# Kernel optimization log

Measured on AMD Instinct MI355X. Metric: run time of the kernel, lower is better.

The kernel has to match this reference:

```python
import jax, jax.numpy as jnp
import numpy as np

B, DIM, NUM_HEADS = 16384, 2048, 4
SD = DIM // 2            # single_dim = 1024
HD = SD // NUM_HEADS     # head_dim = 256
LH = SD // 4             # lambda-net hidden = 256
SCALE = HD ** -0.5


def setup_inputs() -> dict:
    key = jax.random.key(0)
    ks = jax.random.split(key, 20)
    w = lambda k, shape: jax.random.normal(k, shape, dtype=jnp.float32) * 0.02
    inp = {
        "x": jax.random.normal(ks[0], (B, DIM), dtype=jnp.float32),
        # Linear weights stored (in, out); y = x @ W + b (equivalent to torch Linear)
        "WQ1_w": w(ks[1], (SD, SD)), "WQ1_b": jnp.zeros((SD,), jnp.float32),
        "WK1_w": w(ks[2], (SD, SD)), "WK1_b": jnp.zeros((SD,), jnp.float32),
        "WQ2_w": w(ks[3], (SD, SD)), "WQ2_b": jnp.zeros((SD,), jnp.float32),
        "WK2_w": w(ks[4], (SD, SD)), "WK2_b": jnp.zeros((SD,), jnp.float32),
        "WV_w": w(ks[5], (SD, SD)), "WV_b": jnp.zeros((SD,), jnp.float32),
        "WO_w": w(ks[6], (SD, SD)), "WO_b": jnp.zeros((SD,), jnp.float32),
        "L1_w": w(ks[7], (DIM, LH)), "L1_b": jnp.zeros((LH,), jnp.float32),
        "L2_w": w(ks[8], (LH, 1)), "L2_b": jnp.zeros((1,), jnp.float32),
    }
    return inp


def _heads(t, W, b):
    # tokens [B,2,SD] -> [B,H,2,HD]
    y = t @ W + b
    return y.reshape(B, 2, NUM_HEADS, HD).transpose(0, 2, 1, 3)


def reference(x, WQ1_w, WQ1_b, WK1_w, WK1_b, WQ2_w, WQ2_b, WK2_w, WK2_b,
              WV_w, WV_b, WO_w, WO_b, L1_w, L1_b, L2_w, L2_b):
    tokens = x.reshape(B, 2, SD)
    # gating lambda in (0,1): MLP(x) -> [B,1,1,1]
    lam = jax.nn.sigmoid(jax.nn.relu(x @ L1_w + L1_b) @ L2_w + L2_b)
    lam = lam.reshape(B, 1, 1, 1)

    Q1 = _heads(tokens, WQ1_w, WQ1_b)
    K1 = _heads(tokens, WK1_w, WK1_b)
    Q2 = _heads(tokens, WQ2_w, WQ2_b)
    K2 = _heads(tokens, WK2_w, WK2_b)
    V = _heads(tokens, WV_w, WV_b)

    attn1 = jax.nn.softmax(jnp.einsum("bhqd,bhkd->bhqk", Q1, K1) * SCALE, axis=-1)
    attn2 = jax.nn.softmax(jnp.einsum("bhqd,bhkd->bhqk", Q2, K2) * SCALE, axis=-1)
    diff_attn = jax.nn.relu(attn1 - lam * attn2)  # dropout = identity (eval)

    out = jnp.einsum("bhqk,bhkd->bhqd", diff_attn, V)  # [B,H,2,HD]
    out = out.transpose(0, 2, 1, 3).reshape(B, 2, SD)
    out = (out @ WO_w + WO_b) + tokens
    return out.reshape(B, SD * 2)
```

## Files before the change

kernel.cpp:

```cpp
#include <hip/hip_runtime.h>
#include <stdint.h>


#define BATCH  16384
#define ATT_SCALE 0.0625f

typedef __attribute__((ext_vector_type(8)))  short   s16x8;
typedef __attribute__((ext_vector_type(4)))  float   f32x4;
typedef __attribute__((ext_vector_type(2)))  float   f32x2;
typedef __attribute__((ext_vector_type(8)))  int     i32x8;
typedef __attribute__((ext_vector_type(8)))  unsigned short u16x8;
typedef __attribute__((ext_vector_type(4)))  unsigned short u16x4;

__device__ __forceinline__ unsigned short f2bf(float f) {
  unsigned u = __float_as_uint(f);
  u += 0x7FFFu + ((u >> 16) & 1u);
  return (unsigned short)(u >> 16);
}
__device__ __forceinline__ float bf2f(unsigned short s) {
  return __uint_as_float((unsigned)s << 16);
}

__device__ __forceinline__ unsigned char f2e4m3(float f) {
  unsigned u = __float_as_uint(f);
  unsigned s = (u >> 24) & 0x80u;
  float a = fabsf(f);
  if (a >= 448.f) return (unsigned char)(s | 0x7E);
  if (a < 0.0009765625f) return (unsigned char)s;
  int e = (int)((u >> 23) & 0xFF) - 127;
  if (e < -6) {
    int q = (int)rintf(a * 512.f);
    if (q >= 8) return (unsigned char)(s | 0x08);
    return (unsigned char)(s | q);
  }
  unsigned mant = u & 0x7FFFFFu;
  unsigned mr = mant + 0x7FFFFu + ((mant >> 20) & 1u);
  e += (int)(mr >> 23);
  mant = (mr >> 20) & 7u;
  if (e > 8) return (unsigned char)(s | 0x7E);
  return (unsigned char)(s | ((e + 7) << 3) | mant);
}
__device__ __forceinline__ float e4m3f(unsigned v) {
  unsigned e = (v >> 3) & 15u, m = v & 7u;
  float mag = (e == 0) ? (float)m * 0.001953125f
                       : __uint_as_float(((e + 120u) << 23) | (m << 20));
  return (v & 0x80u) ? -mag : mag;
}

__device__ __forceinline__ unsigned char cvt1_fp8(float v) {
#if __has_builtin(__builtin_amdgcn_cvt_pk_fp8_f32)
  return (unsigned char)(__builtin_amdgcn_cvt_pk_fp8_f32(v, v, 0, false) & 0xff);
#else
  return f2e4m3(v);
#endif
}

__device__ __forceinline__ void dec8(uint2 p, float* o) {
#if __has_builtin(__builtin_amdgcn_cvt_pk_f32_fp8)
  f32x2 a = __builtin_amdgcn_cvt_pk_f32_fp8((int)p.x, false);
  f32x2 b = __builtin_amdgcn_cvt_pk_f32_fp8((int)p.x, true);
  f32x2 c = __builtin_amdgcn_cvt_pk_f32_fp8((int)p.y, false);
  f32x2 d = __builtin_amdgcn_cvt_pk_f32_fp8((int)p.y, true);
  o[0] = a[0]; o[1] = a[1]; o[2] = b[0]; o[3] = b[1];
  o[4] = c[0]; o[5] = c[1]; o[6] = d[0]; o[7] = d[1];
#else
#pragma unroll
  for (int j = 0; j < 4; ++j) o[j]     = e4m3f((p.x >> (8 * j)) & 255u);
#pragma unroll
  for (int j = 0; j < 4; ++j) o[4 + j] = e4m3f((p.y >> (8 * j)) & 255u);
#endif
}

__device__ __forceinline__ void async16(const void* g, void* l) {
  __builtin_amdgcn_global_load_lds((__attribute__((address_space(1))) void*)g,
                                   (__attribute__((address_space(3))) void*)l,
                                   16, 0, 0);
}

__global__ __launch_bounds__(512, 2)
void gemm_mx(const unsigned char* __restrict__ A,
             const unsigned char* __restrict__ Bt,
             const float* __restrict__ bias,
             unsigned char* __restrict__ Cout,
             int NN)
{
  __shared__ __align__(16) char lds[131072];
  const int tid  = threadIdx.x;
  const int lane = tid & 63, w = tid >> 6;
  const int wm = w >> 2, wn = w & 3;
  const int li = lane & 15, lc = lane >> 4;

  const int nwg = gridDim.x;
  const int swz = (blockIdx.x & 7) * (nwg >> 3) + (blockIdx.x >> 3);
  const int bm = (swz / NN) * 256;
  const int bn = (swz % NN) * 256;

  const int grow   = lane >> 3;
  const int gchunk = ((lane & 7) ^ grow) * 16;
  size_t aSrc[4], bSrc[4];
  int dstKB[4];
#pragma unroll
  for (int i = 0; i < 4; ++i) {
    const int rr = (i * 8 + w) * 8 + grow;
    aSrc[i] = (size_t)(bm + rr) * 1024 + gchunk;
    bSrc[i] = (size_t)(bn + rr) * 1024 + gchunk;
    dstKB[i] = (i * 8 + w) * 1024;
  }

  const int x7   = li & 7;
  const int off0 = ((2 * lc)     ^ x7) * 16;
  const int off1 = ((2 * lc + 1) ^ x7) * 16;
  const int aRow = (wm * 128 + li) * 128;
  const int bRow = 32768 + (wn * 64 + li) * 128;

  f32x4 acc[8][4];
#pragma unroll
  for (int m = 0; m < 8; ++m)
#pragma unroll
    for (int n = 0; n < 4; ++n) acc[m][n] = (f32x4)0.f;

#pragma unroll
  for (int i = 0; i < 4; ++i) {
    async16(A  + aSrc[i], lds + dstKB[i]);
    async16(Bt + bSrc[i], lds + 32768 + dstKB[i]);
  }
#pragma unroll
  for (int i = 0; i < 4; ++i) {
    async16(A  + aSrc[i] + 128, lds + 65536 + dstKB[i]);
    async16(Bt + bSrc[i] + 128, lds + 98304 + dstKB[i]);
  }
  asm volatile("s_waitcnt vmcnt(8)" ::: "memory");
  __builtin_amdgcn_s_barrier();

  for (int t = 0; t < 8; ++t) {
    char* buf = lds + (t & 1) * 65536;
    const char* ab = buf;
    const char* bb = buf;

    i32x8 bF[4];
#pragma unroll
    for (int nf = 0; nf < 4; ++nf) {
      const char* p = bb + bRow + nf * 2048;
      uint4 h0 = *(const uint4*)(p + off0);
      uint4 h1 = *(const uint4*)(p + off1);
      bF[nf][0] = h0.x; bF[nf][1] = h0.y; bF[nf][2] = h0.z; bF[nf][3] = h0.w;
      bF[nf][4] = h1.x; bF[nf][5] = h1.y; bF[nf][6] = h1.z; bF[nf][7] = h1.w;
    }
#pragma unroll
    for (int mh = 0; mh < 2; ++mh) {
      i32x8 aF[4];
#pragma unroll
      for (int mf = 0; mf < 4; ++mf) {
        const char* p = ab + aRow + (mh * 4 + mf) * 2048;
        uint4 h0 = *(const uint4*)(p + off0);
        uint4 h1 = *(const uint4*)(p + off1);
        aF[mf][0] = h0.x; aF[mf][1] = h0.y; aF[mf][2] = h0.z; aF[mf][3] = h0.w;
        aF[mf][4] = h1.x; aF[mf][5] = h1.y; aF[mf][6] = h1.z; aF[mf][7] = h1.w;
      }
      __builtin_amdgcn_s_setprio(1);
#pragma unroll
      for (int mf = 0; mf < 4; ++mf)
#pragma unroll
        for (int nf = 0; nf < 4; ++nf)
          acc[mh * 4 + mf][nf] = __builtin_amdgcn_mfma_scale_f32_16x16x128_f8f6f4(
              aF[mf], bF[nf], acc[mh * 4 + mf][nf],
              0, 0,
              0, 0x7F7F7F7F,
              0, 0x7F7F7F7F);
      __builtin_amdgcn_s_setprio(0);
    }
    __builtin_amdgcn_s_barrier();
    if (t + 2 < 8) {
      const size_t kt = (size_t)(t + 2) * 128;
#pragma unroll
      for (int i = 0; i < 4; ++i) {
        async16(A  + aSrc[i] + kt, buf + dstKB[i]);
        async16(Bt + bSrc[i] + kt, buf + 32768 + dstKB[i]);
      }
    }
    if (t < 6) { asm volatile("s_waitcnt vmcnt(8)" ::: "memory"); }
    else       { asm volatile("s_waitcnt vmcnt(0)" ::: "memory"); }
    __builtin_amdgcn_s_barrier();
  }

  float bv[4];
#pragma unroll
  for (int n = 0; n < 4; ++n) bv[n] = bias[bn + wn * 64 + n * 16 + li];

  unsigned char* wl0 = (unsigned char*)(lds + w * 12288);
#pragma unroll
  for (int mp = 0; mp < 4; ++mp) {
    unsigned char* wl = wl0 + (mp & 1) * 2560;
#pragma unroll
    for (int mi = 0; mi < 2; ++mi)
#pragma unroll
      for (int n = 0; n < 4; ++n)
#pragma unroll
        for (int jj = 0; jj < 4; ++jj) {
          float v = acc[mp * 2 + mi][n][jj] + bv[n];
          wl[(mi * 16 + lc * 4 + jj) * 80 + n * 16 + li] = cvt1_fp8(v);
        }
    const size_t base = (size_t)((bm + wm * 128 + mp * 32) >> 5) * 131072
                      + (size_t)((bn >> 6) + wn) * 2048;
    uint4 v0 = *(const uint4*)(wl + (lane >> 2) * 80 + (lane & 3) * 16);
    *(uint4*)(Cout + base + lane * 16) = v0;
    uint4 v1 = *(const uint4*)(wl + (16 + (lane >> 2)) * 80 + (lane & 3) * 16);
    *(uint4*)(Cout + base + 1024 + lane * 16) = v1;
  }
}

template<int MODE>
__global__ __launch_bounds__(512, 2)
void gemm256(const unsigned short* __restrict__ A,
             const unsigned short* __restrict__ Bt,
             const float* __restrict__ bias,
             void* __restrict__ Cout,
             const unsigned short* __restrict__ res,
             int Kdim, int Ndim, int NN,
             const unsigned short* __restrict__ lamBt,
             const float* __restrict__ lamL1b,
             const float* __restrict__ lamL2w,
             float* __restrict__ lamp)
{
  __shared__ __align__(16) char lds[131072];
  const int tid  = threadIdx.x;
  const int lane = tid & 63, w = tid >> 6;
  const int wm = w >> 2, wn = w & 3;
  const int li = lane & 15, lc = lane >> 4;

  if (MODE == 4 && blockIdx.x < 128) {
    const int bm_l = blockIdx.x * 128;
    const int t = tid;
    const size_t aSrc  = (size_t)(bm_l + (t >> 2)) * 2048 + (t & 3) * 8;
    const size_t b0Src = (size_t)(t >> 2) * 2048 + (t & 3) * 8;
    const size_t b1Src = (size_t)(128 + (t >> 2)) * 2048 + (t & 3) * 8;

    f32x4 acc[4][4];
#pragma unroll
    for (int i = 0; i < 4; ++i)
#pragma unroll
      for (int j = 0; j < 4; ++j) acc[i][j] = (f32x4)0.f;

    for (int k0 = 0; k0 < 2048; k0 += 32) {
      async16(A     + aSrc  + k0, lds + w * 1024);
      async16(lamBt + b0Src + k0, lds + 8192 + w * 1024);
      async16(lamBt + b1Src + k0, lds + 16384 + w * 1024);
      __syncthreads();
      s16x8 aR[4], bR[4];
#pragma unroll
      for (int m = 0; m < 4; ++m)
        aR[m] = *(const s16x8*)(lds + ((w >> 2) * 64 + m * 16 + li) * 64 + lc * 16);
#pragma unroll
      for (int n = 0; n < 4; ++n)
        bR[n] = *(const s16x8*)(lds + 8192 + ((w & 3) * 64 + n * 16 + li) * 64 + lc * 16);
#pragma unroll
      for (int m = 0; m < 4; ++m)
#pragma unroll
        for (int n = 0; n < 4; ++n)
          acc[m][n] = __builtin_amdgcn_mfma_f32_16x16x32_bf16(aR[m], bR[n], acc[m][n], 0, 0, 0);
      __syncthreads();
    }

    float l2v[4], bvv[4];
#pragma unroll
    for (int n = 0; n < 4; ++n) {
      const int col = (w & 3) * 64 + n * 16 + li;
      l2v[n] = lamL2w[col];
      bvv[n] = lamL1b[col];
    }
#pragma unroll
    for (int m = 0; m < 4; ++m)
#pragma unroll
      for (int j = 0; j < 4; ++j) {
        float part = 0.f;
#pragma unroll
        for (int n = 0; n < 4; ++n)
          part += fmaxf(acc[m][n][j] + bvv[n], 0.f) * l2v[n];
        part += __shfl_xor(part, 1, 64);
        part += __shfl_xor(part, 2, 64);
        part += __shfl_xor(part, 4, 64);
        part += __shfl_xor(part, 8, 64);
        if ((lane & 15) == 0)
          atomicAdd(lamp + bm_l + (w >> 2) * 64 + m * 16 + lc * 4 + j, part);
      }
    return;
  }

  int bid, nwg;
  if (MODE == 4) { bid = blockIdx.x - 128; nwg = 512; }
  else           { bid = blockIdx.x;       nwg = gridDim.x; }
  const int q8 = nwg >> 3, r8 = nwg & 7;
  const int xcd = bid & 7, pos = bid >> 3;
  const int swz = (xcd < r8 ? xcd * (q8 + 1) : r8 * (q8 + 1) + (xcd - r8) * q8) + pos;
  const int bm = (swz / NN) * 256;
  const int bn = (swz % NN) * 256;

  const int r0  = w * 32 + (lane >> 2);
  const int csw = ((lane & 3) ^ ((r0 >> 1) & 3)) * 8;
  const size_t aS0 = (size_t)(bm + r0) * Kdim + csw;
  const size_t aS1 = (size_t)(bm + r0 + 16) * Kdim + csw;
  const size_t bS0 = (size_t)(bn + r0) * Kdim + csw;
  const size_t bS1 = (size_t)(bn + r0 + 16) * Kdim + csw;
  const int dL0 = w * 2048, dL1 = dL0 + 1024;

  const int fsw   = (lc ^ ((li >> 1) & 3)) << 4;
  const int afoff = (wm * 128 + li) * 64 + fsw;
  const int bfoff = 32768 + (wn * 64 + li) * 64 + fsw;

  f32x4 acc[8][4];
#pragma unroll
  for (int m = 0; m < 8; ++m)
#pragma unroll
    for (int n = 0; n < 4; ++n) acc[m][n] = (f32x4)0.f;

  const int NT = Kdim >> 6;

  async16(A  + aS0,       lds + dL0);          async16(A  + aS1,       lds + dL1);
  async16(Bt + bS0,       lds + 32768 + dL0);  async16(Bt + bS1,       lds + 32768 + dL1);
  async16(A  + aS0 + 32,  lds + 16384 + dL0);  async16(A  + aS1 + 32,  lds + 16384 + dL1);
  async16(Bt + bS0 + 32,  lds + 49152 + dL0);  async16(Bt + bS1 + 32,  lds + 49152 + dL1);
  async16(A  + aS0 + 64,  lds + 65536 + dL0);  async16(A  + aS1 + 64,  lds + 65536 + dL1);
  async16(Bt + bS0 + 64,  lds + 98304 + dL0);  async16(Bt + bS1 + 64,  lds + 98304 + dL1);
  asm volatile("s_waitcnt vmcnt(4)" ::: "memory");
  __builtin_amdgcn_s_barrier();

  for (int t = 0; t < NT; ++t) {
    char* buf  = lds + (t & 1) * 65536;
    char* nbuf = lds + ((t + 1) & 1) * 65536;
    const size_t kA = (size_t)t * 64;
    const bool s1 = (t + 1 < NT), s2 = (t + 2 < NT);
    s16x8 a0[4], a1[4], bR[4];

    {
      const char* ab = buf + afoff;
      const char* bb = buf + bfoff;
#pragma unroll
      for (int i = 0; i < 4; ++i) a0[i] = *(const s16x8*)(ab + i * 1024);
#pragma unroll
      for (int i = 0; i < 4; ++i) a1[i] = *(const s16x8*)(ab + 4096 + i * 1024);
#pragma unroll
      for (int i = 0; i < 4; ++i) bR[i] = *(const s16x8*)(bb + i * 1024);
      if (s1) {
        async16(A  + aS0 + kA + 96, nbuf + 16384 + dL0);
        async16(A  + aS1 + kA + 96, nbuf + 16384 + dL1);
        async16(Bt + bS0 + kA + 96, nbuf + 49152 + dL0);
        async16(Bt + bS1 + kA + 96, nbuf + 49152 + dL1);
      }
      __builtin_amdgcn_s_setprio(1);
#pragma unroll
      for (int mf = 0; mf < 4; ++mf)
#pragma unroll
        for (int nf = 0; nf < 4; ++nf) {
          acc[mf][nf]     = __builtin_amdgcn_mfma_f32_16x16x32_bf16(a0[mf], bR[nf], acc[mf][nf], 0, 0, 0);
          acc[4 + mf][nf] = __builtin_amdgcn_mfma_f32_16x16x32_bf16(a1[mf], bR[nf], acc[4 + mf][nf], 0, 0, 0);
        }
      __builtin_amdgcn_s_setprio(0);
      __builtin_amdgcn_s_barrier();
    }
    {
      const char* ab = buf + 16384 + afoff;
      const char* bb = buf + 16384 + bfoff;
#pragma unroll
      for (int i = 0; i < 4; ++i) a0[i] = *(const s16x8*)(ab + i * 1024);
#pragma unroll
      for (int i = 0; i < 4; ++i) a1[i] = *(const s16x8*)(ab + 4096 + i * 1024);
#pragma unroll
      for (int i = 0; i < 4; ++i) bR[i] = *(const s16x8*)(bb + i * 1024);
      if (s2) {
        async16(A  + aS0 + kA + 128, buf + dL0);
        async16(A  + aS1 + kA + 128, buf + dL1);
        async16(Bt + bS0 + kA + 128, buf + 32768 + dL0);
        async16(Bt + bS1 + kA + 128, buf + 32768 + dL1);
      }
      __builtin_amdgcn_s_setprio(1);
#pragma unroll
      for (int mf = 0; mf < 4; ++mf)
#pragma unroll
        for (int nf = 0; nf < 4; ++nf) {
          acc[mf][nf]     = __builtin_amdgcn_mfma_f32_16x16x32_bf16(a0[mf], bR[nf], acc[mf][nf], 0, 0, 0);
          acc[4 + mf][nf] = __builtin_amdgcn_mfma_f32_16x16x32_bf16(a1[mf], bR[nf], acc[4 + mf][nf], 0, 0, 0);
        }
      __builtin_amdgcn_s_setprio(0);
      if (t < NT - 2)       { asm volatile("s_waitcnt vmcnt(4)" ::: "memory"); }
      else if (t == NT - 2) { asm volatile("s_waitcnt vmcnt(0)" ::: "memory"); }
      __builtin_amdgcn_s_barrier();
    }
  }

  float bv[4];
#pragma unroll
  for (int n = 0; n < 4; ++n) bv[n] = bias[bn + wn * 64 + n * 16 + li];

  if (MODE == 4) {
    unsigned short* Cv = (unsigned short*)Cout;
    unsigned short* wl0 = (unsigned short*)(lds + w * 12288);
#pragma unroll
    for (int mp = 0; mp < 4; ++mp) {
      unsigned short* wl = wl0 + (mp & 1) * 2304;
#pragma unroll
      for (int mi = 0; mi < 2; ++mi)
#pragma unroll
        for (int n = 0; n < 4; ++n)
#pragma unroll
          for (int jj = 0; jj < 4; ++jj) {
            float v = acc[mp * 2 + mi][n][jj] + bv[n];
            wl[(mi * 16 + lc * 4 + jj) * 72 + li + n * 16] = f2bf(v);
          }
#pragma unroll
      for (int i = 0; i < 4; ++i) {
        const int rr = i * 8 + (lane >> 3);
        u16x8 vv = *(const u16x8*)(wl + rr * 72 + (lane & 7) * 8);
        const size_t gi = (size_t)(bm + wm * 128 + mp * 32 + rr) * 1024
                        + bn + wn * 64 + (lane & 7) * 8;
        *(u16x8*)(Cv + gi) = vv;
      }
    }
  } else {
    float* Cf = (float*)Cout;
    float* wl0 = (float*)(lds + w * 12288);
#pragma unroll
    for (int m = 0; m < 8; ++m) {
      float* wl = wl0 + (m & 1) * 1088;
#pragma unroll
      for (int n = 0; n < 4; ++n)
#pragma unroll
        for (int jj = 0; jj < 4; ++jj)
          wl[(lc * 4 + jj) * 68 + li + n * 16] = acc[m][n][jj] + bv[n];
#pragma unroll
      for (int i = 0; i < 4; ++i) {
        const int rr = i * 4 + lc;
        f32x4 vv = *(const f32x4*)(wl + rr * 68 + li * 4);
        const size_t gi = (size_t)(bm + wm * 128 + m * 16 + rr) * Ndim
                        + bn + wn * 64 + li * 4;
        const u16x4 rv = *(const u16x4*)(res + gi);
        f32x4 ov;
#pragma unroll
        for (int jj = 0; jj < 4; ++jj) ov[jj] = vv[jj] + bf2f(rv[jj]);
        *(f32x4*)(Cf + gi) = ov;
      }
    }
  }
}

__global__ __launch_bounds__(256)
void attn_kernel(const unsigned char* __restrict__ qk8,
                 const unsigned short* __restrict__ vbuf,
                 const float* __restrict__ lam_pre,
                 const float* __restrict__ L2b,
                 unsigned short* __restrict__ aout)
{
  const int b = blockIdx.x;
  const int hd = threadIdx.x >> 6;
  const int lane = threadIdx.x & 63;
  const int g = lane >> 5;
  const int l5 = lane & 31;
  const size_t row = (size_t)(2 * b + g);

  const size_t cbase = (row >> 5) * 131072
                     + (size_t)(hd * 4 + (l5 >> 3)) * 2048
                     + (row & 31) * 64 + (l5 & 7) * 8;
  const uint2 p1 = *(const uint2*)(qk8 + cbase);
  const uint2 p2 = *(const uint2*)(qk8 + cbase + 32768);
  const uint2 p3 = *(const uint2*)(qk8 + cbase + 65536);
  const uint2 p4 = *(const uint2*)(qk8 + cbase + 98304);
  const u16x8 vvv = *(const u16x8*)(vbuf + row * 1024 + hd * 256 + l5 * 8);

  float q1[8], k1[8], q2[8], k2[8], vf[8];
  dec8(p1, q1); dec8(p2, k1); dec8(p3, q2); dec8(p4, k2);
#pragma unroll
  for (int j = 0; j < 8; ++j) vf[j] = bf2f(vvv[j]);

  float ss1 = 0.f, sc1 = 0.f, ss2 = 0.f, sc2 = 0.f;
#pragma unroll
  for (int j = 0; j < 8; ++j) {
    const float k1o = __shfl_xor(k1[j], 32, 64);
    const float k2o = __shfl_xor(k2[j], 32, 64);
    ss1 += q1[j] * k1[j]; sc1 += q1[j] * k1o;
    ss2 += q2[j] * k2[j]; sc2 += q2[j] * k2o;
  }
#pragma unroll
  for (int m = 16; m >= 1; m >>= 1) {
    ss1 += __shfl_xor(ss1, m, 64); sc1 += __shfl_xor(sc1, m, 64);
    ss2 += __shfl_xor(ss2, m, 64); sc2 += __shfl_xor(sc2, m, 64);
  }

  float e0 = ss1 * ATT_SCALE, e1 = sc1 * ATT_SCALE;
  float mx = fmaxf(e0, e1);
  float xs = expf(e0 - mx), xc = expf(e1 - mx);
  float inv = 1.f / (xs + xc);
  const float a1s = xs * inv, a1c = xc * inv;

  e0 = ss2 * ATT_SCALE; e1 = sc2 * ATT_SCALE;
  mx = fmaxf(e0, e1);
  xs = expf(e0 - mx); xc = expf(e1 - mx);
  inv = 1.f / (xs + xc);
  const float a2s = xs * inv, a2c = xc * inv;

  const float lm = 1.f / (1.f + expf(-(lam_pre[b] + L2b[0])));
  const float ps = fmaxf(a1s - lm * a2s, 0.f);
  const float pc = fmaxf(a1c - lm * a2c, 0.f);

  u16x8 o;
#pragma unroll
  for (int j = 0; j < 8; ++j) {
    const float vo = __shfl_xor(vf[j], 32, 64);
    o[j] = f2bf(ps * vf[j] + pc * vo);
  }
  *(u16x8*)(aout + row * 1024 + hd * 256 + l5 * 8) = o;
}

__global__ void prep_k(const float* __restrict__ s0, const float* __restrict__ s1,
                       const float* __restrict__ s2, const float* __restrict__ s3,
                       const float* __restrict__ s4, const float* __restrict__ s5,
                       const float* __restrict__ L1w,
                       const float* __restrict__ b0, const float* __restrict__ b1,
                       const float* __restrict__ b2, const float* __restrict__ b3,
                       const float* __restrict__ b4,
                       const float* __restrict__ x,
                       unsigned char* __restrict__ qw8,
                       unsigned short* __restrict__ vw,
                       unsigned short* __restrict__ wot,
                       unsigned short* __restrict__ l1t,
                       float* __restrict__ bcat,
                       unsigned short* __restrict__ x_bf,
                       unsigned char* __restrict__ x_f8,
                       float* __restrict__ lamp)
{
  __shared__ float tile[32][33];
  const int z = blockIdx.z;
  const int tx = threadIdx.x, ty = threadIdx.y;

  if (z < 6) {
    const float* W;
    switch (z) {
      case 0: W = s0; break;
      case 1: W = s1; break;
      case 2: W = s2; break;
      case 3: W = s3; break;
      case 4: W = s4; break;
      default: W = s5; break;
    }
    const int bn = blockIdx.x * 32, bk = blockIdx.y * 32;
#pragma unroll
    for (int i = ty; i < 32; i += 8)
      tile[i][tx] = W[(size_t)(bk + i) * 1024 + bn + tx];
    __syncthreads();
    if (z < 4) {
      unsigned char* Wt = qw8 + (size_t)z * 1048576;
#pragma unroll
      for (int i = ty; i < 32; i += 8)
        Wt[(size_t)(bn + i) * 1024 + bk + tx] = cvt1_fp8(tile[tx][i]);
    } else {
      unsigned short* Wt = (z == 4) ? vw : wot;
#pragma unroll
      for (int i = ty; i < 32; i += 8)
        Wt[(size_t)(bn + i) * 1024 + bk + tx] = f2bf(tile[tx][i]);
    }
    return;
  }
  if (z < 22) {
    const int c = (z - 6) * 1024 + blockIdx.y * 32 + blockIdx.x;
    const int i = c * 256 + ty * 32 + tx;
    const float4* p = (const float4*)x + (size_t)i * 2;
    float4 a = p[0], b = p[1];
    float f[8] = {a.x, a.y, a.z, a.w, b.x, b.y, b.z, b.w};
    u16x8 v; unsigned lo = 0, hi = 0;
#pragma unroll
    for (int j = 0; j < 8; ++j) v[j] = f2bf(f[j]);
#pragma unroll
    for (int j = 0; j < 4; ++j) lo |= (unsigned)cvt1_fp8(f[j]) << (8 * j);
#pragma unroll
    for (int j = 0; j < 4; ++j) hi |= (unsigned)cvt1_fp8(f[4 + j]) << (8 * j);
    *(u16x8*)(x_bf + (size_t)i * 8) = v;
    uint2 c8; c8.x = lo; c8.y = hi;
    *(uint2*)(x_f8 + (size_t)i * 8) = c8;
    return;
  }
  if (z == 22) {
    const int idx = blockIdx.y * 32 + blockIdx.x;
    if (idx >= 512) return;
    const int bn = (idx & 7) * 32, bk = (idx >> 3) * 32;
#pragma unroll
    for (int i = ty; i < 32; i += 8)
      tile[i][tx] = L1w[(size_t)(bk + i) * 256 + bn + tx];
    __syncthreads();
#pragma unroll
    for (int i = ty; i < 32; i += 8)
      l1t[(size_t)(bn + i) * 2048 + bk + tx] = f2bf(tile[tx][i]);
    return;
  }
  const int idx = blockIdx.y * 32 + blockIdx.x;
  const int t = ty * 32 + tx;
  if (idx < 20) {
    const int i = idx * 256 + t;
    const float* src;
    switch (i >> 10) {
      case 0: src = b0; break;
      case 1: src = b1; break;
      case 2: src = b2; break;
      case 3: src = b3; break;
      default: src = b4; break;
    }
    bcat[i] = src[i & 1023];
  } else if (idx < 84) {
    lamp[(idx - 20) * 256 + t] = 0.f;
  }
}

extern "C" void kernel_launch(void* const* d_in, const int* in_sizes, int n_in,
                              void* d_out, int out_size, void* d_ws, size_t ws_size,
                              hipStream_t stream)
{
  const float* x    = (const float*)d_in[0];
  const float* WQ1w = (const float*)d_in[1];  const float* WQ1b = (const float*)d_in[2];
  const float* WK1w = (const float*)d_in[3];  const float* WK1b = (const float*)d_in[4];
  const float* WQ2w = (const float*)d_in[5];  const float* WQ2b = (const float*)d_in[6];
  const float* WK2w = (const float*)d_in[7];  const float* WK2b = (const float*)d_in[8];
  const float* WVw  = (const float*)d_in[9];  const float* WVb  = (const float*)d_in[10];
  const float* WOw  = (const float*)d_in[11]; const float* WOb  = (const float*)d_in[12];
  const float* L1w  = (const float*)d_in[13]; const float* L1b  = (const float*)d_in[14];
  const float* L2w  = (const float*)d_in[15]; const float* L2b  = (const float*)d_in[16];

  char* ws = (char*)d_ws;
  size_t off = 0;
  unsigned short* x_bf = (unsigned short*)(ws + off); off += (size_t)33554432 * 2;
  unsigned char*  x_f8 = (unsigned char*)(ws + off);  off += (size_t)33554432;
  unsigned char*  qw8  = (unsigned char*)(ws + off);  off += (size_t)4194304;
  unsigned short* vw   = (unsigned short*)(ws + off); off += (size_t)1048576 * 2;
  unsigned short* wot  = (unsigned short*)(ws + off); off += (size_t)1048576 * 2;
  unsigned short* l1t  = (unsigned short*)(ws + off); off += (size_t)524288 * 2;
  float*          bcat = (float*)(ws + off);          off += (size_t)5120 * 4;
  unsigned char*  qk8  = (unsigned char*)(ws + off);  off += (size_t)32768 * 4096;
  unsigned short* vbuf = (unsigned short*)(ws + off); off += (size_t)33554432 * 2;
  unsigned short* abuf = (unsigned short*)(ws + off); off += (size_t)33554432 * 2;
  float*          lamp = (float*)(ws + off);          off += (size_t)16384 * 4;

  prep_k<<<dim3(32, 32, 24), dim3(32, 8), 0, stream>>>(
      WQ1w, WK1w, WQ2w, WK2w, WVw, WOw, L1w,
      WQ1b, WK1b, WQ2b, WK2b, WVb, x,
      qw8, vw, wot, l1t, bcat, x_bf, x_f8, lamp);

  gemm_mx<<<dim3(2048), 512, 0, stream>>>(x_f8, qw8, bcat, qk8, 16);

  gemm256<4><<<dim3(128 + 512), 512, 0, stream>>>(
      x_bf, vw, bcat + 4096, vbuf, nullptr, 1024, 1024, 4, l1t, L1b, L2w, lamp);

  attn_kernel<<<16384, 256, 0, stream>>>(qk8, vbuf, lamp, L2b, abuf);

  gemm256<2><<<dim3(512), 512, 0, stream>>>(
      abuf, wot, WOb, d_out, x_bf, 1024, 1024, 4, nullptr, nullptr, nullptr, nullptr);
}
```

Before: 467.9 us.

## Compute V projection in FP8 MFMA, merged into QK GEMM launch with lambda net

The V projection weight is now quantized to FP8 with the Q/K weights, so V comes out of the same FP8 scaled-MFMA GEMM as Q1/K1/Q2/K2 (N widened from 4096 to 5120), written back as bf16. The lambda-MLP blocks move into this combined launch, which drops one kernel launch and replaces the bf16 V GEMM with the cheaper FP8 path. In exchange V loses precision from FP8 inputs, which may hurt accuracy. The output projection becomes its own non-templated kernel.

```diff
diff --git a/kernel.cpp b/kernel.cpp
--- a/kernel.cpp
+++ b/kernel.cpp
@@ -82,141 +82,9 @@
              const unsigned char* __restrict__ Bt,
              const float* __restrict__ bias,
              unsigned char* __restrict__ Cout,
-             int NN)
-{
-  __shared__ __align__(16) char lds[131072];
-  const int tid  = threadIdx.x;
-  const int lane = tid & 63, w = tid >> 6;
-  const int wm = w >> 2, wn = w & 3;
-  const int li = lane & 15, lc = lane >> 4;
-
-  const int nwg = gridDim.x;
-  const int swz = (blockIdx.x & 7) * (nwg >> 3) + (blockIdx.x >> 3);
-  const int bm = (swz / NN) * 256;
-  const int bn = (swz % NN) * 256;
-
-  const int grow   = lane >> 3;
-  const int gchunk = ((lane & 7) ^ grow) * 16;
-  size_t aSrc[4], bSrc[4];
-  int dstKB[4];
-#pragma unroll
-  for (int i = 0; i < 4; ++i) {
-    const int rr = (i * 8 + w) * 8 + grow;
-    aSrc[i] = (size_t)(bm + rr) * 1024 + gchunk;
-    bSrc[i] = (size_t)(bn + rr) * 1024 + gchunk;
-    dstKB[i] = (i * 8 + w) * 1024;
-  }
-
-  const int x7   = li & 7;
-  const int off0 = ((2 * lc)     ^ x7) * 16;
-  const int off1 = ((2 * lc + 1) ^ x7) * 16;
-  const int aRow = (wm * 128 + li) * 128;
-  const int bRow = 32768 + (wn * 64 + li) * 128;
-
-  f32x4 acc[8][4];
-#pragma unroll
-  for (int m = 0; m < 8; ++m)
-#pragma unroll
-    for (int n = 0; n < 4; ++n) acc[m][n] = (f32x4)0.f;
-
-#pragma unroll
-  for (int i = 0; i < 4; ++i) {
-    async16(A  + aSrc[i], lds + dstKB[i]);
-    async16(Bt + bSrc[i], lds + 32768 + dstKB[i]);
-  }
-#pragma unroll
-  for (int i = 0; i < 4; ++i) {
-    async16(A  + aSrc[i] + 128, lds + 65536 + dstKB[i]);
-    async16(Bt + bSrc[i] + 128, lds + 98304 + dstKB[i]);
-  }
-  asm volatile("s_waitcnt vmcnt(8)" ::: "memory");
-  __builtin_amdgcn_s_barrier();
-
-  for (int t = 0; t < 8; ++t) {
-    char* buf = lds + (t & 1) * 65536;
-    const char* ab = buf;
-    const char* bb = buf;
-
-    i32x8 bF[4];
-#pragma unroll
-    for (int nf = 0; nf < 4; ++nf) {
-      const char* p = bb + bRow + nf * 2048;
-      uint4 h0 = *(const uint4*)(p + off0);
-      uint4 h1 = *(const uint4*)(p + off1);
-      bF[nf][0] = h0.x; bF[nf][1] = h0.y; bF[nf][2] = h0.z; bF[nf][3] = h0.w;
-      bF[nf][4] = h1.x; bF[nf][5] = h1.y; bF[nf][6] = h1.z; bF[nf][7] = h1.w;
-    }
-#pragma unroll
-    for (int mh = 0; mh < 2; ++mh) {
-      i32x8 aF[4];
-#pragma unroll
-      for (int mf = 0; mf < 4; ++mf) {
-        const char* p = ab + aRow + (mh * 4 + mf) * 2048;
-        uint4 h0 = *(const uint4*)(p + off0);
-        uint4 h1 = *(const uint4*)(p + off1);
-        aF[mf][0] = h0.x; aF[mf][1] = h0.y; aF[mf][2] = h0.z; aF[mf][3] = h0.w;
-        aF[mf][4] = h1.x; aF[mf][5] = h1.y; aF[mf][6] = h1.z; aF[mf][7] = h1.w;
-      }
-      __builtin_amdgcn_s_setprio(1);
-#pragma unroll
-      for (int mf = 0; mf < 4; ++mf)
-#pragma unroll
-        for (int nf = 0; nf < 4; ++nf)
-          acc[mh * 4 + mf][nf] = __builtin_amdgcn_mfma_scale_f32_16x16x128_f8f6f4(
-              aF[mf], bF[nf], acc[mh * 4 + mf][nf],
-              0, 0,
-              0, 0x7F7F7F7F,
-              0, 0x7F7F7F7F);
-      __builtin_amdgcn_s_setprio(0);
-    }
-    __builtin_amdgcn_s_barrier();
-    if (t + 2 < 8) {
-      const size_t kt = (size_t)(t + 2) * 128;
-#pragma unroll
-      for (int i = 0; i < 4; ++i) {
-        async16(A  + aSrc[i] + kt, buf + dstKB[i]);
-        async16(Bt + bSrc[i] + kt, buf + 32768 + dstKB[i]);
-      }
-    }
-    if (t < 6) { asm volatile("s_waitcnt vmcnt(8)" ::: "memory"); }
-    else       { asm volatile("s_waitcnt vmcnt(0)" ::: "memory"); }
-    __builtin_amdgcn_s_barrier();
-  }
-
-  float bv[4];
-#pragma unroll
-  for (int n = 0; n < 4; ++n) bv[n] = bias[bn + wn * 64 + n * 16 + li];
-
-  unsigned char* wl0 = (unsigned char*)(lds + w * 12288);
-#pragma unroll
-  for (int mp = 0; mp < 4; ++mp) {
-    unsigned char* wl = wl0 + (mp & 1) * 2560;
-#pragma unroll
-    for (int mi = 0; mi < 2; ++mi)
-#pragma unroll
-      for (int n = 0; n < 4; ++n)
-#pragma unroll
-        for (int jj = 0; jj < 4; ++jj) {
-          float v = acc[mp * 2 + mi][n][jj] + bv[n];
-          wl[(mi * 16 + lc * 4 + jj) * 80 + n * 16 + li] = cvt1_fp8(v);
-        }
-    const size_t base = (size_t)((bm + wm * 128 + mp * 32) >> 5) * 131072
-                      + (size_t)((bn >> 6) + wn) * 2048;
-    uint4 v0 = *(const uint4*)(wl + (lane >> 2) * 80 + (lane & 3) * 16);
-    *(uint4*)(Cout + base + lane * 16) = v0;
-    uint4 v1 = *(const uint4*)(wl + (16 + (lane >> 2)) * 80 + (lane & 3) * 16);
-    *(uint4*)(Cout + base + 1024 + lane * 16) = v1;
-  }
-}
-
-template<int MODE>
-__global__ __launch_bounds__(512, 2)
-void gemm256(const unsigned short* __restrict__ A,
-             const unsigned short* __restrict__ Bt,
-             const float* __restrict__ bias,
-             void* __restrict__ Cout,
-             const unsigned short* __restrict__ res,
-             int Kdim, int Ndim, int NN,
+             unsigned short* __restrict__ Vout,
+             int NN,
+             const unsigned short* __restrict__ xbf,
              const unsigned short* __restrict__ lamBt,
              const float* __restrict__ lamL1b,
              const float* __restrict__ lamL2w,
@@ -228,7 +96,7 @@
   const int wm = w >> 2, wn = w & 3;
   const int li = lane & 15, lc = lane >> 4;
 
-  if (MODE == 4 && blockIdx.x < 128) {
+  if (blockIdx.x < 128) {
     const int bm_l = blockIdx.x * 128;
     const int t = tid;
     const size_t aSrc  = (size_t)(bm_l + (t >> 2)) * 2048 + (t & 3) * 8;
@@ -242,7 +110,7 @@
       for (int j = 0; j < 4; ++j) acc[i][j] = (f32x4)0.f;
 
     for (int k0 = 0; k0 < 2048; k0 += 32) {
-      async16(A     + aSrc  + k0, lds + w * 1024);
+      async16(xbf   + aSrc  + k0, lds + w * 1024);
       async16(lamBt + b0Src + k0, lds + 8192 + w * 1024);
       async16(lamBt + b1Src + k0, lds + 16384 + w * 1024);
       __syncthreads();
@@ -286,11 +154,165 @@
     return;
   }
 
-  int bid, nwg;
-  if (MODE == 4) { bid = blockIdx.x - 128; nwg = 512; }
-  else           { bid = blockIdx.x;       nwg = gridDim.x; }
+  const int bid = blockIdx.x - 128;
+  const int nwg = 2560;
+  const int swz = (bid & 7) * (nwg >> 3) + (bid >> 3);
+  const int bm = (swz / NN) * 256;
+  const int bn = (swz % NN) * 256;
+
+  const int grow   = lane >> 3;
+  const int gchunk = ((lane & 7) ^ grow) * 16;
+  size_t aSrc[4], bSrc[4];
+  int dstKB[4];
+#pragma unroll
+  for (int i = 0; i < 4; ++i) {
+    const int rr = (i * 8 + w) * 8 + grow;
+    aSrc[i] = (size_t)(bm + rr) * 1024 + gchunk;
+    bSrc[i] = (size_t)(bn + rr) * 1024 + gchunk;
+    dstKB[i] = (i * 8 + w) * 1024;
+  }
+
+  const int x7   = li & 7;
+  const int off0 = ((2 * lc)     ^ x7) * 16;
+  const int off1 = ((2 * lc + 1) ^ x7) * 16;
+  const int aRow = (wm * 128 + li) * 128;
+  const int bRow = 32768 + (wn * 64 + li) * 128;
+
+  f32x4 acc[8][4];
+#pragma unroll
+  for (int m = 0; m < 8; ++m)
+#pragma unroll
+    for (int n = 0; n < 4; ++n) acc[m][n] = (f32x4)0.f;
+
+#pragma unroll
+  for (int i = 0; i < 4; ++i) {
+    async16(A  + aSrc[i], lds + dstKB[i]);
+    async16(Bt + bSrc[i], lds + 32768 + dstKB[i]);
+  }
+#pragma unroll
+  for (int i = 0; i < 4; ++i) {
+    async16(A  + aSrc[i] + 128, lds + 65536 + dstKB[i]);
+    async16(Bt + bSrc[i] + 128, lds + 98304 + dstKB[i]);
+  }
+  asm volatile("s_waitcnt vmcnt(8)" ::: "memory");
+  __builtin_amdgcn_s_barrier();
+
+  for (int t = 0; t < 8; ++t) {
+    char* buf = lds + (t & 1) * 65536;
+
+    i32x8 bF[4];
+#pragma unroll
+    for (int nf = 0; nf < 4; ++nf) {
+      const char* p = buf + bRow + nf * 2048;
+      uint4 h0 = *(const uint4*)(p + off0);
+      uint4 h1 = *(const uint4*)(p + off1);
+      bF[nf][0] = h0.x; bF[nf][1] = h0.y; bF[nf][2] = h0.z; bF[nf][3] = h0.w;
+      bF[nf][4] = h1.x; bF[nf][5] = h1.y; bF[nf][6] = h1.z; bF[nf][7] = h1.w;
+    }
+#pragma unroll
+    for (int mh = 0; mh < 2; ++mh) {
+      i32x8 aF[4];
+#pragma unroll
+      for (int mf = 0; mf < 4; ++mf) {
+        const char* p = buf + aRow + (mh * 4 + mf) * 2048;
+        uint4 h0 = *(const uint4*)(p + off0);
+        uint4 h1 = *(const uint4*)(p + off1);
+        aF[mf][0] = h0.x; aF[mf][1] = h0.y; aF[mf][2] = h0.z; aF[mf][3] = h0.w;
+        aF[mf][4] = h1.x; aF[mf][5] = h1.y; aF[mf][6] = h1.z; aF[mf][7] = h1.w;
+      }
+      __builtin_amdgcn_s_setprio(1);
+#pragma unroll
+      for (int mf = 0; mf < 4; ++mf)
+#pragma unroll
+        for (int nf = 0; nf < 4; ++nf)
+          acc[mh * 4 + mf][nf] = __builtin_amdgcn_mfma_scale_f32_16x16x128_f8f6f4(
+              aF[mf], bF[nf], acc[mh * 4 + mf][nf],
+              0, 0, 0, 0x7F7F7F7F, 0, 0x7F7F7F7F);
+      __builtin_amdgcn_s_setprio(0);
+    }
+    __builtin_amdgcn_s_barrier();
+    if (t + 2 < 8) {
+      const size_t kt = (size_t)(t + 2) * 128;
+#pragma unroll
+      for (int i = 0; i < 4; ++i) {
+        async16(A  + aSrc[i] + kt, buf + dstKB[i]);
+        async16(Bt + bSrc[i] + kt, buf + 32768 + dstKB[i]);
+      }
+    }
+    if (t < 6) { asm volatile("s_waitcnt vmcnt(8)" ::: "memory"); }
+    else       { asm volatile("s_waitcnt vmcnt(0)" ::: "memory"); }
+    __builtin_amdgcn_s_barrier();
+  }
+
+  float bv[4];
+#pragma unroll
+  for (int n = 0; n < 4; ++n) bv[n] = bias[bn + wn * 64 + n * 16 + li];
+
+  if (bn < 4096) {
+    unsigned char* wl0 = (unsigned char*)(lds + w * 12288);
+#pragma unroll
+    for (int mp = 0; mp < 4; ++mp) {
+      unsigned char* wl = wl0 + (mp & 1) * 2560;
+#pragma unroll
+      for (int mi = 0; mi < 2; ++mi)
+#pragma unroll
+        for (int n = 0; n < 4; ++n)
+#pragma unroll
+          for (int jj = 0; jj < 4; ++jj) {
+            float v = acc[mp * 2 + mi][n][jj] + bv[n];
+            wl[(mi * 16 + lc * 4 + jj) * 80 + n * 16 + li] = cvt1_fp8(v);
+          }
+      const size_t base = (size_t)((bm + wm * 128 + mp * 32) >> 5) * 131072
+                        + (size_t)((bn >> 6) + wn) * 2048;
+      uint4 v0 = *(const uint4*)(wl + (lane >> 2) * 80 + (lane & 3) * 16);
+      *(uint4*)(Cout + base + lane * 16) = v0;
+      uint4 v1 = *(const uint4*)(wl + (16 + (lane >> 2)) * 80 + (lane & 3) * 16);
+      *(uint4*)(Cout + base + 1024 + lane * 16) = v1;
+    }
+  } else {
+    unsigned short* wl0 = (unsigned short*)(lds + w * 12288);
+    const int cb = bn - 4096;
+#pragma unroll
+    for (int mp = 0; mp < 4; ++mp) {
+      unsigned short* wl = wl0 + (mp & 1) * 2304;
+#pragma unroll
+      for (int mi = 0; mi < 2; ++mi)
+#pragma unroll
+        for (int n = 0; n < 4; ++n)
+#pragma unroll
+          for (int jj = 0; jj < 4; ++jj) {
+            float v = acc[mp * 2 + mi][n][jj] + bv[n];
+            wl[(mi * 16 + lc * 4 + jj) * 72 + li + n * 16] = f2bf(v);
+          }
+#pragma unroll
+      for (int i = 0; i < 4; ++i) {
+        const int rr = i * 8 + (lane >> 3);
+        u16x8 vv = *(const u16x8*)(wl + rr * 72 + (lane & 7) * 8);
+        const size_t gi = (size_t)(bm + wm * 128 + mp * 32 + rr) * 1024
+                        + cb + wn * 64 + (lane & 7) * 8;
+        *(u16x8*)(Vout + gi) = vv;
+      }
+    }
+  }
+}
+
+__global__ __launch_bounds__(512, 2)
+void gemm_wo(const unsigned short* __restrict__ A,
+             const unsigned short* __restrict__ Bt,
+             const float* __restrict__ bias,
+             float* __restrict__ Cout,
+             const unsigned short* __restrict__ res,
+             int Kdim, int Ndim, int NN)
+{
+  __shared__ __align__(16) char lds[131072];
+  const int tid  = threadIdx.x;
+  const int lane = tid & 63, w = tid >> 6;
+  const int wm = w >> 2, wn = w & 3;
+  const int li = lane & 15, lc = lane >> 4;
+
+  const int nwg = gridDim.x;
   const int q8 = nwg >> 3, r8 = nwg & 7;
-  const int xcd = bid & 7, pos = bid >> 3;
+  const int xcd = blockIdx.x & 7, pos = blockIdx.x >> 3;
   const int swz = (xcd < r8 ? xcd * (q8 + 1) : r8 * (q8 + 1) + (xcd - r8) * q8) + pos;
   const int bm = (swz / NN) * 256;
   const int bn = (swz % NN) * 256;
@@ -391,53 +413,26 @@
 #pragma unroll
   for (int n = 0; n < 4; ++n) bv[n] = bias[bn + wn * 64 + n * 16 + li];
 
-  if (MODE == 4) {
-    unsigned short* Cv = (unsigned short*)Cout;
-    unsigned short* wl0 = (unsigned short*)(lds + w * 12288);
-#pragma unroll
-    for (int mp = 0; mp < 4; ++mp) {
-      unsigned short* wl = wl0 + (mp & 1) * 2304;
-#pragma unroll
-      for (int mi = 0; mi < 2; ++mi)
-#pragma unroll
-        for (int n = 0; n < 4; ++n)
-#pragma unroll
-          for (int jj = 0; jj < 4; ++jj) {
-            float v = acc[mp * 2 + mi][n][jj] + bv[n];
-            wl[(mi * 16 + lc * 4 + jj) * 72 + li + n * 16] = f2bf(v);
-          }
-#pragma unroll
-      for (int i = 0; i < 4; ++i) {
-        const int rr = i * 8 + (lane >> 3);
-        u16x8 vv = *(const u16x8*)(wl + rr * 72 + (lane & 7) * 8);
-        const size_t gi = (size_t)(bm + wm * 128 + mp * 32 + rr) * 1024
-                        + bn + wn * 64 + (lane & 7) * 8;
-        *(u16x8*)(Cv + gi) = vv;
-      }
-    }
-  } else {
-    float* Cf = (float*)Cout;
-    float* wl0 = (float*)(lds + w * 12288);
-#pragma unroll
-    for (int m = 0; m < 8; ++m) {
-      float* wl = wl0 + (m & 1) * 1088;
-#pragma unroll
-      for (int n = 0; n < 4; ++n)
-#pragma unroll
-        for (int jj = 0; jj < 4; ++jj)
-          wl[(lc * 4 + jj) * 68 + li + n * 16] = acc[m][n][jj] + bv[n];
-#pragma unroll
-      for (int i = 0; i < 4; ++i) {
-        const int rr = i * 4 + lc;
-        f32x4 vv = *(const f32x4*)(wl + rr * 68 + li * 4);
-        const size_t gi = (size_t)(bm + wm * 128 + m * 16 + rr) * Ndim
-                        + bn + wn * 64 + li * 4;
-        const u16x4 rv = *(const u16x4*)(res + gi);
-        f32x4 ov;
-#pragma unroll
-        for (int jj = 0; jj < 4; ++jj) ov[jj] = vv[jj] + bf2f(rv[jj]);
-        *(f32x4*)(Cf + gi) = ov;
-      }
+  float* wl0 = (float*)(lds + w * 12288);
+#pragma unroll
+  for (int m = 0; m < 8; ++m) {
+    float* wl = wl0 + (m & 1) * 1088;
+#pragma unroll
+    for (int n = 0; n < 4; ++n)
+#pragma unroll
+      for (int jj = 0; jj < 4; ++jj)
+        wl[(lc * 4 + jj) * 68 + li + n * 16] = acc[m][n][jj] + bv[n];
+#pragma unroll
+    for (int i = 0; i < 4; ++i) {
+      const int rr = i * 4 + lc;
+      f32x4 vv = *(const f32x4*)(wl + rr * 68 + li * 4);
+      const size_t gi = (size_t)(bm + wm * 128 + m * 16 + rr) * Ndim
+                      + bn + wn * 64 + li * 4;
+      const u16x4 rv = *(const u16x4*)(res + gi);
+      f32x4 ov;
+#pragma unroll
+      for (int jj = 0; jj < 4; ++jj) ov[jj] = vv[jj] + bf2f(rv[jj]);
+      *(f32x4*)(Cout + gi) = ov;
     }
   }
 }
@@ -518,7 +513,6 @@
                        const float* __restrict__ b4,
                        const float* __restrict__ x,
                        unsigned char* __restrict__ qw8,
-                       unsigned short* __restrict__ vw,
                        unsigned short* __restrict__ wot,
                        unsigned short* __restrict__ l1t,
                        float* __restrict__ bcat,
@@ -545,16 +539,15 @@
     for (int i = ty; i < 32; i += 8)
       tile[i][tx] = W[(size_t)(bk + i) * 1024 + bn + tx];
     __syncthreads();
-    if (z < 4) {
+    if (z < 5) {
       unsigned char* Wt = qw8 + (size_t)z * 1048576;
 #pragma unroll
       for (int i = ty; i < 32; i += 8)
         Wt[(size_t)(bn + i) * 1024 + bk + tx] = cvt1_fp8(tile[tx][i]);
     } else {
-      unsigned short* Wt = (z == 4) ? vw : wot;
 #pragma unroll
       for (int i = ty; i < 32; i += 8)
-        Wt[(size_t)(bn + i) * 1024 + bk + tx] = f2bf(tile[tx][i]);
+        wot[(size_t)(bn + i) * 1024 + bk + tx] = f2bf(tile[tx][i]);
     }
     return;
   }
@@ -625,8 +618,7 @@
   size_t off = 0;
   unsigned short* x_bf = (unsigned short*)(ws + off); off += (size_t)33554432 * 2;
   unsigned char*  x_f8 = (unsigned char*)(ws + off);  off += (size_t)33554432;
-  unsigned char*  qw8  = (unsigned char*)(ws + off);  off += (size_t)4194304;
-  unsigned short* vw   = (unsigned short*)(ws + off); off += (size_t)1048576 * 2;
+  unsigned char*  qw8  = (unsigned char*)(ws + off);  off += (size_t)5242880;
   unsigned short* wot  = (unsigned short*)(ws + off); off += (size_t)1048576 * 2;
   unsigned short* l1t  = (unsigned short*)(ws + off); off += (size_t)524288 * 2;
   float*          bcat = (float*)(ws + off);          off += (size_t)5120 * 4;
@@ -638,15 +630,13 @@
   prep_k<<<dim3(32, 32, 24), dim3(32, 8), 0, stream>>>(
       WQ1w, WK1w, WQ2w, WK2w, WVw, WOw, L1w,
       WQ1b, WK1b, WQ2b, WK2b, WVb, x,
-      qw8, vw, wot, l1t, bcat, x_bf, x_f8, lamp);
-
-  gemm_mx<<<dim3(2048), 512, 0, stream>>>(x_f8, qw8, bcat, qk8, 16);
-
-  gemm256<4><<<dim3(128 + 512), 512, 0, stream>>>(
-      x_bf, vw, bcat + 4096, vbuf, nullptr, 1024, 1024, 4, l1t, L1b, L2w, lamp);
+      qw8, wot, l1t, bcat, x_bf, x_f8, lamp);
+
+  gemm_mx<<<dim3(128 + 2560), 512, 0, stream>>>(
+      x_f8, qw8, bcat, qk8, vbuf, 20, x_bf, l1t, L1b, L2w, lamp);
 
   attn_kernel<<<16384, 256, 0, stream>>>(qk8, vbuf, lamp, L2b, abuf);
 
-  gemm256<2><<<dim3(512), 512, 0, stream>>>(
-      abuf, wot, WOb, d_out, x_bf, 1024, 1024, 4, nullptr, nullptr, nullptr, nullptr);
-}
+  gemm_wo<<<dim3(512), 512, 0, stream>>>(
+      abuf, wot, WOb, (float*)d_out, x_bf, 1024, 1024, 4);
+}
```

After: 428.7 us. 1.09x faster.
